# Optimization experiments

Measured on AMD Instinct MI355X. Metric: run time of the kernel, lower is better.

## Reference

```python
import jax, jax.numpy as jnp
import numpy as np

N, DIN, DOUT = 8192, 4096, 4096

def setup_inputs() -> dict:
    key = jax.random.key(0)
    k1, k2 = jax.random.split(key)
    x = jax.random.normal(k1, (N, DIN), dtype=jnp.float32)
    # ternary-ish weights; forward applies sign() via STE anyway
    weight = jax.random.normal(k2, (DOUT, DIN), dtype=jnp.float32)
    bias = jnp.zeros((DOUT,), dtype=jnp.float32)
    scale = jnp.ones((1,), dtype=jnp.float32)  # scale_init = 1.0
    return {"x": x, "weight": weight, "bias": bias, "scale": scale}


def reference(x, weight, bias, scale):
    # STE sign-quantization: value is sign(weight) in {-1,0,1},
    # gradient flows to weight as identity.
    w = weight - jax.lax.stop_gradient(weight - jnp.sign(weight))
    # fused ternary matmul + scale + bias: out = scale * (x @ w.T + bias)
    # (backward in the torch code scales grad for x, w, AND bias, implying
    #  bias sits inside the scale multiplier)
    return scale[0] * (jnp.matmul(x, w.T) + bias)
```

## Files before the change

kernel.cpp:

```cpp
#include <hip/hip_runtime.h>
#include <hip/hip_bf16.h>
#include <stdint.h>

#define M_DIM 8192
#define K_DIM 4096
#define N_DIM 4096

typedef int intx4  __attribute__((ext_vector_type(4)));
typedef int intx16 __attribute__((ext_vector_type(16)));

__global__ void __launch_bounds__(512)
cvt_fused_i8_kernel(const float* __restrict__ x,
                    const float* __restrict__ w,
                    signed char* __restrict__ xb,
                    signed char* __restrict__ wb,
                    float* __restrict__ row_scale) {
    const int b   = blockIdx.x;
    const int tid = threadIdx.x;
    if (b < 1024) {
        const int wv   = tid >> 6;
        const int lane = tid & 63;
        const int row  = b * 8 + wv;
        const float* xr = x + (size_t)row * K_DIM;

        float am = 0.f;
#pragma unroll
        for (int i = 0; i < 16; ++i) {
            const float4 v = *(const float4*)(xr + lane * 4 + i * 256);
            am = fmaxf(am, fmaxf(fmaxf(fabsf(v.x), fabsf(v.y)),
                                 fmaxf(fabsf(v.z), fabsf(v.w))));
        }
#pragma unroll
        for (int off = 32; off > 0; off >>= 1)
            am = fmaxf(am, __shfl_xor(am, off));
        am = fmaxf(am, 1e-30f);
        const float inv = 127.f / am;

        signed char* xo = xb + (size_t)row * K_DIM;
#pragma unroll
        for (int i = 0; i < 16; ++i) {
            const float4 v = *(const float4*)(xr + lane * 4 + i * 256);
            const float vf[4] = {v.x, v.y, v.z, v.w};
            union { signed char c[4]; uint32_t u; } r;
#pragma unroll
            for (int k = 0; k < 4; ++k) {
                int q = (int)rintf(vf[k] * inv);
                q = q > 127 ? 127 : (q < -127 ? -127 : q);
                r.c[k] = (signed char)q;
            }
            *(uint32_t*)(xo + lane * 4 + i * 256) = r.u;
        }
        if (lane == 0) row_scale[row] = am * (1.f / 127.f);
    } else {
        const int bw = b - 1024;
        const size_t t0 = (size_t)bw * 512 + tid;
#pragma unroll
        for (int i = 0; i < 4; ++i) {
            const size_t idx = t0 + (size_t)i * 1048576;
            const float4 a = *(const float4*)(w + idx * 4);
            union { signed char s[4]; uint32_t u; } r;
            r.s[0] = (a.x > 0.f) - (a.x < 0.f);
            r.s[1] = (a.y > 0.f) - (a.y < 0.f);
            r.s[2] = (a.z > 0.f) - (a.z < 0.f);
            r.s[3] = (a.w > 0.f) - (a.w < 0.f);
            *(uint32_t*)(wb + idx * 4) = r.u;
        }
    }
}

__device__ __forceinline__ void gld_lds16(const void* g, void* l) {
    __builtin_amdgcn_global_load_lds(
        (const __attribute__((address_space(1))) void*)g,
        (__attribute__((address_space(3))) void*)l,
        16, 0, 0);
}

__global__ void __launch_bounds__(512, 2)
gemm_i8_kernel(const signed char* __restrict__ A,
               const signed char* __restrict__ B,
               const float* __restrict__ bias,
               const float* __restrict__ scale,
               const float* __restrict__ row_scale,
               float* __restrict__ out) {
    __shared__ __attribute__((aligned(16))) signed char sA[3][256 * 64];
    __shared__ __attribute__((aligned(16))) signed char sB[3][256 * 64];

    const int tid  = threadIdx.x;
    const int lane = tid & 63;
    const int wave = tid >> 6;
    const int wm = wave >> 2;
    const int wn = wave & 3;
    const int r5 = lane & 31;
    const int hi = lane >> 5;

    const int bid = blockIdx.x;
    const int swz = (bid & 7) * 64 + (bid >> 3);
    const int rowBase = (swz >> 4) * 256;
    const int colBase = (swz & 15) * 256;

    const int sc   = (lane & 3) ^ ((lane >> 3) & 3) ^ ((wave & 1) << 1);
    const int srow = wave * 16 + (lane >> 2);
    const signed char* gA0 = A + (size_t)(rowBase + srow) * K_DIM + sc * 16;
    const signed char* gA1 = gA0 + (size_t)128 * K_DIM;
    const signed char* gB0 = B + (size_t)(colBase + srow) * K_DIM + sc * 16;
    const signed char* gB1 = gB0 + (size_t)128 * K_DIM;
    const int ldsR0 = wave * 1024;
    const int ldsR1 = 8192 + wave * 1024;

    const int fsw = ((r5 >> 1) & 3) ^ (((r5 >> 4) & 1) << 1);
    const int ckE = ((hi + 0) ^ fsw) * 16;
    const int ckO = ((hi + 2) ^ fsw) * 16;
    const int aOff = (wm * 128 + r5) * 64;
    const int bOff = (wn * 64 + r5) * 64;

    intx16 acc[4][2] = {};

#pragma unroll
    for (int s = 0; s < 2; ++s) {
        const size_t kg = (size_t)s * 64;
        gld_lds16(gA0 + kg, &sA[s][ldsR0]);
        gld_lds16(gA1 + kg, &sA[s][ldsR1]);
        gld_lds16(gB0 + kg, &sB[s][ldsR0]);
        gld_lds16(gB1 + kg, &sB[s][ldsR1]);
    }
    asm volatile("s_waitcnt vmcnt(4)" ::: "memory");
    __builtin_amdgcn_s_barrier();

    int sr = 0;
    int sw = 2;
    for (int t = 0; t < 64; ++t) {
        const signed char* sAb = sA[sr];
        const signed char* sBb = sB[sr];

        intx4 fa[4], fb[2];
#pragma unroll
        for (int mt = 0; mt < 4; ++mt)
            fa[mt] = *(const intx4*)(sAb + aOff + mt * 2048 + ckE);
#pragma unroll
        for (int nt = 0; nt < 2; ++nt)
            fb[nt] = *(const intx4*)(sBb + bOff + nt * 2048 + ckE);
        __builtin_amdgcn_sched_barrier(0);

        intx4 oa[4], ob[2];
#pragma unroll
        for (int mt = 0; mt < 4; ++mt)
            oa[mt] = *(const intx4*)(sAb + aOff + mt * 2048 + ckO);
#pragma unroll
        for (int nt = 0; nt < 2; ++nt)
            ob[nt] = *(const intx4*)(sBb + bOff + nt * 2048 + ckO);
        if (t <= 61) {
            const size_t kg = (size_t)(t + 2) * 64;
            gld_lds16(gA0 + kg, &sA[sw][ldsR0]);
            gld_lds16(gA1 + kg, &sA[sw][ldsR1]);
            gld_lds16(gB0 + kg, &sB[sw][ldsR0]);
            gld_lds16(gB1 + kg, &sB[sw][ldsR1]);
        }
        __builtin_amdgcn_sched_barrier(0);

        __builtin_amdgcn_s_setprio(1);
#pragma unroll
        for (int mt = 0; mt < 4; ++mt)
#pragma unroll
            for (int nt = 0; nt < 2; ++nt)
                acc[mt][nt] = __builtin_amdgcn_mfma_i32_32x32x32_i8(
                    fa[mt], fb[nt], acc[mt][nt], 0, 0, 0);
        __builtin_amdgcn_s_setprio(0);
        __builtin_amdgcn_sched_barrier(0);

        __builtin_amdgcn_s_setprio(1);
#pragma unroll
        for (int mt = 0; mt < 4; ++mt)
#pragma unroll
            for (int nt = 0; nt < 2; ++nt)
                acc[mt][nt] = __builtin_amdgcn_mfma_i32_32x32x32_i8(
                    oa[mt], ob[nt], acc[mt][nt], 0, 0, 0);
        __builtin_amdgcn_s_setprio(0);
        __builtin_amdgcn_sched_barrier(0);

        if (t <= 61)      asm volatile("s_waitcnt vmcnt(4)" ::: "memory");
        else if (t == 62) asm volatile("s_waitcnt vmcnt(0)" ::: "memory");
        __builtin_amdgcn_s_barrier();

        sr = (sr == 2) ? 0 : sr + 1;
        sw = (sw == 2) ? 0 : sw + 1;
    }

    const float s = scale[0];
#pragma unroll
    for (int nt = 0; nt < 2; ++nt) {
        const int gcol = colBase + wn * 64 + nt * 32 + r5;
        const float bv = bias[gcol];
#pragma unroll
        for (int mt = 0; mt < 4; ++mt) {
#pragma unroll
            for (int q = 0; q < 4; ++q) {
                const int row0 = rowBase + wm * 128 + mt * 32 + q * 8 + hi * 4;
                const float4 rs4 = *(const float4*)(row_scale + row0);
                const float rs[4] = {rs4.x, rs4.y, rs4.z, rs4.w};
#pragma unroll
                for (int r = 0; r < 4; ++r)
                    __builtin_nontemporal_store(
                        s * ((float)acc[mt][nt][q * 4 + r] * rs[r] + bv),
                        out + (size_t)(row0 + r) * N_DIM + gcol);
            }
        }
    }
}

__global__ void fallback_kernel(const float* __restrict__ x,
                                const float* __restrict__ w,
                                const float* __restrict__ bias,
                                const float* __restrict__ scale,
                                float* __restrict__ out) {
    int col = blockIdx.x * 64 + (threadIdx.x & 63);
    int row = blockIdx.y * 4 + (threadIdx.x >> 6);
    const float* xr = x + (size_t)row * K_DIM;
    const float* wr = w + (size_t)col * K_DIM;
    float acc = 0.f;
    for (int k = 0; k < K_DIM; k += 4) {
        float4 a = *(const float4*)(xr + k);
        float4 b = *(const float4*)(wr + k);
        acc += a.x * (b.x > 0.f ? 1.f : (b.x < 0.f ? -1.f : 0.f));
        acc += a.y * (b.y > 0.f ? 1.f : (b.y < 0.f ? -1.f : 0.f));
        acc += a.z * (b.z > 0.f ? 1.f : (b.z < 0.f ? -1.f : 0.f));
        acc += a.w * (b.w > 0.f ? 1.f : (b.w < 0.f ? -1.f : 0.f));
    }
    out[(size_t)row * N_DIM + col] = scale[0] * (acc + bias[col]);
}

extern "C" void kernel_launch(void* const* d_in, const int* in_sizes, int n_in,
                              void* d_out, int out_size, void* d_ws, size_t ws_size,
                              hipStream_t stream) {
    const float* x     = (const float*)d_in[0];
    const float* w     = (const float*)d_in[1];
    const float* bias  = (const float*)d_in[2];
    const float* scale = (const float*)d_in[3];
    float* out = (float*)d_out;

    const size_t xb_bytes = (size_t)M_DIM * K_DIM;
    const size_t wb_bytes = (size_t)N_DIM * K_DIM;
    const size_t need = xb_bytes + wb_bytes + M_DIM * sizeof(float);

    if (ws_size >= need) {
        signed char* xb = (signed char*)d_ws;
        signed char* wb = xb + xb_bytes;
        float* row_scale = (float*)(wb + wb_bytes);
        cvt_fused_i8_kernel<<<dim3(3072), 512, 0, stream>>>(
            x, w, xb, wb, row_scale);
        gemm_i8_kernel<<<dim3((M_DIM / 256) * (N_DIM / 256)), 512, 0, stream>>>(
            xb, wb, bias, scale, row_scale, out);
    } else {
        dim3 grid(N_DIM / 64, M_DIM / 4);
        fallback_kernel<<<grid, 256, 0, stream>>>(x, w, bias, scale, out);
    }
}
```

Before: 401.2 us.

## Pre-pack int8 operands into MFMA fragment layout and load directly to registers

The conversion kernel now writes quantized x and sign(w) in a tiled layout of 32-row panels, with 16-byte chunks ordered so each lane's MFMA fragment is contiguous. The GEMM drops the LDS triple buffer and barriers and instead loads fragments straight from global memory into registers, double-buffered across two register sets. This removes LDS traffic and workgroup synchronisation. In exchange, operands shared across waves are loaded redundantly from global/L2, which risks higher memory latency exposure and register pressure.

```diff
diff --git a/kernel.cpp b/kernel.cpp
--- a/kernel.cpp
+++ b/kernel.cpp
@@ -8,6 +8,7 @@
 
 typedef int intx4  __attribute__((ext_vector_type(4)));
 typedef int intx16 __attribute__((ext_vector_type(16)));
+
 
 __global__ void __launch_bounds__(512)
 cvt_fused_i8_kernel(const float* __restrict__ x,
@@ -36,43 +37,35 @@
         am = fmaxf(am, 1e-30f);
         const float inv = 127.f / am;
 
-        signed char* xo = xb + (size_t)row * K_DIM;
-#pragma unroll
-        for (int i = 0; i < 16; ++i) {
-            const float4 v = *(const float4*)(xr + lane * 4 + i * 256);
-            const float vf[4] = {v.x, v.y, v.z, v.w};
-            union { signed char c[4]; uint32_t u; } r;
-#pragma unroll
-            for (int k = 0; k < 4; ++k) {
-                int q = (int)rintf(vf[k] * inv);
+        signed char* xo = xb + (size_t)(row >> 5) * 131072 + (row & 31) * 16;
+#pragma unroll
+        for (int i = 0; i < 4; ++i) {
+            const int ch = i * 64 + lane;
+            const float* src = xr + ch * 16;
+            union { signed char c[16]; uint4 u4; } r;
+#pragma unroll
+            for (int j = 0; j < 16; ++j) {
+                int q = (int)rintf(src[j] * inv);
                 q = q > 127 ? 127 : (q < -127 ? -127 : q);
-                r.c[k] = (signed char)q;
+                r.c[j] = (signed char)q;
             }
-            *(uint32_t*)(xo + lane * 4 + i * 256) = r.u;
+            *(uint4*)(xo + (ch >> 1) * 1024 + (ch & 1) * 512) = r.u4;
         }
         if (lane == 0) row_scale[row] = am * (1.f / 127.f);
     } else {
-        const int bw = b - 1024;
-        const size_t t0 = (size_t)bw * 512 + tid;
-#pragma unroll
-        for (int i = 0; i < 4; ++i) {
-            const size_t idx = t0 + (size_t)i * 1048576;
-            const float4 a = *(const float4*)(w + idx * 4);
-            union { signed char s[4]; uint32_t u; } r;
-            r.s[0] = (a.x > 0.f) - (a.x < 0.f);
-            r.s[1] = (a.y > 0.f) - (a.y < 0.f);
-            r.s[2] = (a.z > 0.f) - (a.z < 0.f);
-            r.s[3] = (a.w > 0.f) - (a.w < 0.f);
-            *(uint32_t*)(wb + idx * 4) = r.u;
-        }
-    }
-}
-
-__device__ __forceinline__ void gld_lds16(const void* g, void* l) {
-    __builtin_amdgcn_global_load_lds(
-        (const __attribute__((address_space(1))) void*)g,
-        (__attribute__((address_space(3))) void*)l,
-        16, 0, 0);
+        const size_t gt = (size_t)(b - 1024) * 512 + tid;
+        const int col = (int)(gt >> 8);
+        const int ch  = (int)(gt & 255);
+        const float* src = w + (size_t)col * K_DIM + ch * 16;
+        union { signed char c[16]; uint4 u4; } r;
+#pragma unroll
+        for (int j = 0; j < 16; ++j) {
+            const float a = src[j];
+            r.c[j] = (signed char)((a > 0.f) - (a < 0.f));
+        }
+        *(uint4*)(wb + (size_t)(col >> 5) * 131072 +
+                  (ch >> 1) * 1024 + (ch & 1) * 512 + (col & 31) * 16) = r.u4;
+    }
 }
 
 __global__ void __launch_bounds__(512, 2)
@@ -82,9 +75,6 @@
                const float* __restrict__ scale,
                const float* __restrict__ row_scale,
                float* __restrict__ out) {
-    __shared__ __attribute__((aligned(16))) signed char sA[3][256 * 64];
-    __shared__ __attribute__((aligned(16))) signed char sB[3][256 * 64];
-
     const int tid  = threadIdx.x;
     const int lane = tid & 63;
     const int wave = tid >> 6;
@@ -98,92 +88,61 @@
     const int rowBase = (swz >> 4) * 256;
     const int colBase = (swz & 15) * 256;
 
-    const int sc   = (lane & 3) ^ ((lane >> 3) & 3) ^ ((wave & 1) << 1);
-    const int srow = wave * 16 + (lane >> 2);
-    const signed char* gA0 = A + (size_t)(rowBase + srow) * K_DIM + sc * 16;
-    const signed char* gA1 = gA0 + (size_t)128 * K_DIM;
-    const signed char* gB0 = B + (size_t)(colBase + srow) * K_DIM + sc * 16;
-    const signed char* gB1 = gB0 + (size_t)128 * K_DIM;
-    const int ldsR0 = wave * 1024;
-    const int ldsR1 = 8192 + wave * 1024;
-
-    const int fsw = ((r5 >> 1) & 3) ^ (((r5 >> 4) & 1) << 1);
-    const int ckE = ((hi + 0) ^ fsw) * 16;
-    const int ckO = ((hi + 2) ^ fsw) * 16;
-    const int aOff = (wm * 128 + r5) * 64;
-    const int bOff = (wn * 64 + r5) * 64;
+    const signed char* pA0 =
+        A + (size_t)((rowBase >> 5) + wm * 4) * 131072 + lane * 16;
+    const signed char* pA1 = pA0 + 131072;
+    const signed char* pA2 = pA0 + 2 * 131072;
+    const signed char* pA3 = pA0 + 3 * 131072;
+    const signed char* pB0 =
+        B + (size_t)((colBase >> 5) + wn * 2) * 131072 + lane * 16;
+    const signed char* pB1 = pB0 + 131072;
 
     intx16 acc[4][2] = {};
-
-#pragma unroll
-    for (int s = 0; s < 2; ++s) {
-        const size_t kg = (size_t)s * 64;
-        gld_lds16(gA0 + kg, &sA[s][ldsR0]);
-        gld_lds16(gA1 + kg, &sA[s][ldsR1]);
-        gld_lds16(gB0 + kg, &sB[s][ldsR0]);
-        gld_lds16(gB1 + kg, &sB[s][ldsR1]);
-    }
-    asm volatile("s_waitcnt vmcnt(4)" ::: "memory");
-    __builtin_amdgcn_s_barrier();
-
-    int sr = 0;
-    int sw = 2;
-    for (int t = 0; t < 64; ++t) {
-        const signed char* sAb = sA[sr];
-        const signed char* sBb = sB[sr];
-
-        intx4 fa[4], fb[2];
-#pragma unroll
-        for (int mt = 0; mt < 4; ++mt)
-            fa[mt] = *(const intx4*)(sAb + aOff + mt * 2048 + ckE);
-#pragma unroll
-        for (int nt = 0; nt < 2; ++nt)
-            fb[nt] = *(const intx4*)(sBb + bOff + nt * 2048 + ckE);
-        __builtin_amdgcn_sched_barrier(0);
-
-        intx4 oa[4], ob[2];
-#pragma unroll
-        for (int mt = 0; mt < 4; ++mt)
-            oa[mt] = *(const intx4*)(sAb + aOff + mt * 2048 + ckO);
-#pragma unroll
-        for (int nt = 0; nt < 2; ++nt)
-            ob[nt] = *(const intx4*)(sBb + bOff + nt * 2048 + ckO);
-        if (t <= 61) {
-            const size_t kg = (size_t)(t + 2) * 64;
-            gld_lds16(gA0 + kg, &sA[sw][ldsR0]);
-            gld_lds16(gA1 + kg, &sA[sw][ldsR1]);
-            gld_lds16(gB0 + kg, &sB[sw][ldsR0]);
-            gld_lds16(gB1 + kg, &sB[sw][ldsR1]);
-        }
-        __builtin_amdgcn_sched_barrier(0);
-
-        __builtin_amdgcn_s_setprio(1);
-#pragma unroll
-        for (int mt = 0; mt < 4; ++mt)
-#pragma unroll
-            for (int nt = 0; nt < 2; ++nt)
-                acc[mt][nt] = __builtin_amdgcn_mfma_i32_32x32x32_i8(
-                    fa[mt], fb[nt], acc[mt][nt], 0, 0, 0);
-        __builtin_amdgcn_s_setprio(0);
-        __builtin_amdgcn_sched_barrier(0);
-
-        __builtin_amdgcn_s_setprio(1);
-#pragma unroll
-        for (int mt = 0; mt < 4; ++mt)
-#pragma unroll
-            for (int nt = 0; nt < 2; ++nt)
-                acc[mt][nt] = __builtin_amdgcn_mfma_i32_32x32x32_i8(
-                    oa[mt], ob[nt], acc[mt][nt], 0, 0, 0);
-        __builtin_amdgcn_s_setprio(0);
-        __builtin_amdgcn_sched_barrier(0);
-
-        if (t <= 61)      asm volatile("s_waitcnt vmcnt(4)" ::: "memory");
-        else if (t == 62) asm volatile("s_waitcnt vmcnt(0)" ::: "memory");
-        __builtin_amdgcn_s_barrier();
-
-        sr = (sr == 2) ? 0 : sr + 1;
-        sw = (sw == 2) ? 0 : sw + 1;
-    }
+    intx4 a0[4][2], b0[2][2], a1[4][2], b1[2][2];
+
+#define LOADSET(sa, sb, koff)                                                  \
+    do {                                                                       \
+        sa[0][0] = *(const intx4*)(pA0 + (koff));                              \
+        sa[0][1] = *(const intx4*)(pA0 + (koff) + 1024);                       \
+        sa[1][0] = *(const intx4*)(pA1 + (koff));                              \
+        sa[1][1] = *(const intx4*)(pA1 + (koff) + 1024);                       \
+        sa[2][0] = *(const intx4*)(pA2 + (koff));                              \
+        sa[2][1] = *(const intx4*)(pA2 + (koff) + 1024);                       \
+        sa[3][0] = *(const intx4*)(pA3 + (koff));                              \
+        sa[3][1] = *(const intx4*)(pA3 + (koff) + 1024);                       \
+        sb[0][0] = *(const intx4*)(pB0 + (koff));                              \
+        sb[0][1] = *(const intx4*)(pB0 + (koff) + 1024);                       \
+        sb[1][0] = *(const intx4*)(pB1 + (koff));                              \
+        sb[1][1] = *(const intx4*)(pB1 + (koff) + 1024);                       \
+    } while (0)
+
+#define MFMASET(sa, sb)                                                        \
+    do {                                                                       \
+        __builtin_amdgcn_s_setprio(1);                                         \
+        _Pragma("unroll") for (int ks = 0; ks < 2; ++ks)                       \
+            _Pragma("unroll") for (int mt = 0; mt < 4; ++mt)                   \
+                _Pragma("unroll") for (int nt = 0; nt < 2; ++nt)               \
+                    acc[mt][nt] = __builtin_amdgcn_mfma_i32_32x32x32_i8(       \
+                        sa[mt][ks], sb[nt][ks], acc[mt][nt], 0, 0, 0);         \
+        __builtin_amdgcn_s_setprio(0);                                         \
+    } while (0)
+
+    LOADSET(a0, b0, 0);
+
+#pragma unroll 1
+    for (int i = 0; i < 32; ++i) {
+        const int koff = i * 4096;
+        LOADSET(a1, b1, koff + 2048);
+        __builtin_amdgcn_sched_barrier(0);
+        MFMASET(a0, b0);
+        __builtin_amdgcn_sched_barrier(0);
+        if (i < 31) LOADSET(a0, b0, koff + 4096);
+        __builtin_amdgcn_sched_barrier(0);
+        MFMASET(a1, b1);
+        __builtin_amdgcn_sched_barrier(0);
+    }
+#undef LOADSET
+#undef MFMASET
 
     const float s = scale[0];
 #pragma unroll
```

Result: slower. 449.3 us (+12.0%).

## Software-pipeline LDS fragment loads across k-tiles with ping-pong register buffers

Applied to the files above, without the earlier changes.

Restructures the main K loop so the first half-fragment for the next k-tile is read from LDS between the two MFMA clusters of the current tile. Ping-pong register sets (fa/fb and ga/gb) are used, with the loop unrolled by two. The global-to-LDS prefetch is issued at the start of each tile, and an extra barrier is added after the second cluster. The goal is to hide LDS read latency behind MFMA work, at the cost of more VGPRs and an additional barrier per tile.

```diff
diff --git a/kernel.cpp b/kernel.cpp
--- a/kernel.cpp
+++ b/kernel.cpp
@@ -113,77 +113,89 @@
     const int aOff = (wm * 128 + r5) * 64;
     const int bOff = (wn * 64 + r5) * 64;
 
+    const signed char* sA0 = &sA[0][0];
+    const signed char* sB0 = &sB[0][0];
+
     intx16 acc[4][2] = {};
-
-#pragma unroll
-    for (int s = 0; s < 2; ++s) {
-        const size_t kg = (size_t)s * 64;
-        gld_lds16(gA0 + kg, &sA[s][ldsR0]);
-        gld_lds16(gA1 + kg, &sA[s][ldsR1]);
-        gld_lds16(gB0 + kg, &sB[s][ldsR0]);
-        gld_lds16(gB1 + kg, &sB[s][ldsR1]);
-    }
+    intx4 fa[4], fb[2], ga[4], gb[2], oa[4], ob[2];
+
+#define STAGE(slotB, kt)                                                       \
+    do {                                                                       \
+        const size_t kg_ = (size_t)(kt) * 64;                                  \
+        signed char* pA_ = (signed char*)sA0 + (slotB);                        \
+        signed char* pB_ = (signed char*)sB0 + (slotB);                        \
+        gld_lds16(gA0 + kg_, pA_ + ldsR0);                                     \
+        gld_lds16(gA1 + kg_, pA_ + ldsR1);                                     \
+        gld_lds16(gB0 + kg_, pB_ + ldsR0);                                     \
+        gld_lds16(gB1 + kg_, pB_ + ldsR1);                                     \
+    } while (0)
+
+#define CLUSTER(CA, CB)                                                        \
+    do {                                                                       \
+        __builtin_amdgcn_s_setprio(1);                                         \
+        _Pragma("unroll") for (int mt = 0; mt < 4; ++mt)                       \
+            _Pragma("unroll") for (int nt = 0; nt < 2; ++nt)                   \
+                acc[mt][nt] = __builtin_amdgcn_mfma_i32_32x32x32_i8(           \
+                    CA[mt], CB[nt], acc[mt][nt], 0, 0, 0);                     \
+        __builtin_amdgcn_s_setprio(0);                                         \
+    } while (0)
+
+#define TILE(t, srB, CA, CB, NA, NB)                                           \
+    do {                                                                       \
+        const signed char* sAb = sA0 + (srB);                                  \
+        const signed char* sBb = sB0 + (srB);                                  \
+        if ((t) <= 61) {                                                       \
+            const int swB_ = (srB) >= 16384 ? (srB)-16384 : (srB)+32768;       \
+            STAGE(swB_, (t) + 2);                                              \
+        }                                                                      \
+        _Pragma("unroll") for (int mt = 0; mt < 4; ++mt)                       \
+            oa[mt] = *(const intx4*)(sAb + aOff + mt * 2048 + ckO);            \
+        _Pragma("unroll") for (int nt = 0; nt < 2; ++nt)                       \
+            ob[nt] = *(const intx4*)(sBb + bOff + nt * 2048 + ckO);            \
+        __builtin_amdgcn_sched_barrier(0);                                     \
+        CLUSTER(CA, CB);                                   \
+        __builtin_amdgcn_sched_barrier(0);                                     \
+        if ((t) <= 61)      asm volatile("s_waitcnt vmcnt(4)" ::: "memory");   \
+        else if ((t) == 62) asm volatile("s_waitcnt vmcnt(0)" ::: "memory");   \
+        __builtin_amdgcn_s_barrier();                  \
+        if ((t) < 63) {                                                        \
+            const int nxB_ = (srB) == 32768 ? 0 : (srB) + 16384;               \
+            const signed char* sAn = sA0 + nxB_;                               \
+            const signed char* sBn = sB0 + nxB_;                               \
+            _Pragma("unroll") for (int mt = 0; mt < 4; ++mt)                   \
+                NA[mt] = *(const intx4*)(sAn + aOff + mt * 2048 + ckE);        \
+            _Pragma("unroll") for (int nt = 0; nt < 2; ++nt)                   \
+                NB[nt] = *(const intx4*)(sBn + bOff + nt * 2048 + ckE);        \
+        }                                                                      \
+        __builtin_amdgcn_sched_barrier(0);                                     \
+        CLUSTER(oa, ob);                          \
+        __builtin_amdgcn_sched_barrier(0);                                     \
+        __builtin_amdgcn_s_barrier();                       \
+    } while (0)
+
+    STAGE(0, 0);
+    STAGE(16384, 1);
     asm volatile("s_waitcnt vmcnt(4)" ::: "memory");
     __builtin_amdgcn_s_barrier();
-
-    int sr = 0;
-    int sw = 2;
-    for (int t = 0; t < 64; ++t) {
-        const signed char* sAb = sA[sr];
-        const signed char* sBb = sB[sr];
-
-        intx4 fa[4], fb[2];
-#pragma unroll
-        for (int mt = 0; mt < 4; ++mt)
-            fa[mt] = *(const intx4*)(sAb + aOff + mt * 2048 + ckE);
-#pragma unroll
-        for (int nt = 0; nt < 2; ++nt)
-            fb[nt] = *(const intx4*)(sBb + bOff + nt * 2048 + ckE);
-        __builtin_amdgcn_sched_barrier(0);
-
-        intx4 oa[4], ob[2];
-#pragma unroll
-        for (int mt = 0; mt < 4; ++mt)
-            oa[mt] = *(const intx4*)(sAb + aOff + mt * 2048 + ckO);
-#pragma unroll
-        for (int nt = 0; nt < 2; ++nt)
-            ob[nt] = *(const intx4*)(sBb + bOff + nt * 2048 + ckO);
-        if (t <= 61) {
-            const size_t kg = (size_t)(t + 2) * 64;
-            gld_lds16(gA0 + kg, &sA[sw][ldsR0]);
-            gld_lds16(gA1 + kg, &sA[sw][ldsR1]);
-            gld_lds16(gB0 + kg, &sB[sw][ldsR0]);
-            gld_lds16(gB1 + kg, &sB[sw][ldsR1]);
-        }
-        __builtin_amdgcn_sched_barrier(0);
-
-        __builtin_amdgcn_s_setprio(1);
-#pragma unroll
-        for (int mt = 0; mt < 4; ++mt)
-#pragma unroll
-            for (int nt = 0; nt < 2; ++nt)
-                acc[mt][nt] = __builtin_amdgcn_mfma_i32_32x32x32_i8(
-                    fa[mt], fb[nt], acc[mt][nt], 0, 0, 0);
-        __builtin_amdgcn_s_setprio(0);
-        __builtin_amdgcn_sched_barrier(0);
-
-        __builtin_amdgcn_s_setprio(1);
-#pragma unroll
-        for (int mt = 0; mt < 4; ++mt)
-#pragma unroll
-            for (int nt = 0; nt < 2; ++nt)
-                acc[mt][nt] = __builtin_amdgcn_mfma_i32_32x32x32_i8(
-                    oa[mt], ob[nt], acc[mt][nt], 0, 0, 0);
-        __builtin_amdgcn_s_setprio(0);
-        __builtin_amdgcn_sched_barrier(0);
-
-        if (t <= 61)      asm volatile("s_waitcnt vmcnt(4)" ::: "memory");
-        else if (t == 62) asm volatile("s_waitcnt vmcnt(0)" ::: "memory");
-        __builtin_amdgcn_s_barrier();
-
-        sr = (sr == 2) ? 0 : sr + 1;
-        sw = (sw == 2) ? 0 : sw + 1;
-    }
+#pragma unroll
+    for (int mt = 0; mt < 4; ++mt)
+        fa[mt] = *(const intx4*)(sA0 + aOff + mt * 2048 + ckE);
+#pragma unroll
+    for (int nt = 0; nt < 2; ++nt)
+        fb[nt] = *(const intx4*)(sB0 + bOff + nt * 2048 + ckE);
+
+    int srB = 0;
+#pragma unroll 1
+    for (int tt = 0; tt < 32; ++tt) {
+        const int t0 = tt * 2;
+        TILE(t0,     srB, fa, fb, ga, gb);
+        srB = (srB == 32768) ? 0 : srB + 16384;
+        TILE(t0 + 1, srB, ga, gb, fa, fb);
+        srB = (srB == 32768) ? 0 : srB + 16384;
+    }
+#undef TILE
+#undef CLUSTER
+#undef STAGE
 
     const float s = scale[0];
 #pragma unroll
```

Result: slower. 424.2 us (+5.7%).
